# Performance work log

Measured on AMD Instinct MI355X. Metric: run time of the kernel, lower is better.

The kernel has to match this reference:

```python
import jax, jax.numpy as jnp
import numpy as np

GRID = 10
NV = 6
SD = 4
TSD = NV * SD  # 24
PRED = 5
DT = 0.1
BN_EPS = 1e-5


def _conv(x, w, b):
    y = jax.lax.conv_general_dilated(x, w, (1, 1), 'SAME',
                                     dimension_numbers=('NCHW', 'OIHW', 'NCHW'))
    return y + b[None, :, None, None]


def _pool(x):
    return jax.lax.reduce_window(x, -jnp.inf, jax.lax.max,
                                 (1, 1, 2, 2), (1, 1, 2, 2), 'VALID')


def _bn_eval(x, g, b):
    # eval-mode BatchNorm with running_mean=0, running_var=1
    return g * x / jnp.sqrt(1.0 + BN_EPS) + b


def _lstm(x, Wih, Whh, bih, bhh):
    # x: [B, T, D]; torch gate order i, f, g, o
    B = x.shape[0]
    H = Whh.shape[1]
    def step(carry, xt):
        h, c = carry
        gates = xt @ Wih.T + h @ Whh.T + bih + bhh
        i, f, g, o = jnp.split(gates, 4, axis=-1)
        c = jax.nn.sigmoid(f) * c + jax.nn.sigmoid(i) * jnp.tanh(g)
        h = jax.nn.sigmoid(o) * jnp.tanh(c)
        return (h, c), h
    init = (jnp.zeros((B, H), x.dtype), jnp.zeros((B, H), x.dtype))
    (h, c), ys = jax.lax.scan(step, init, jnp.swapaxes(x, 0, 1))
    return jnp.swapaxes(ys, 0, 1), (h, c)


def setup_inputs() -> dict:
    key = jax.random.key(0)
    B, T, D = 512, 100, 400
    C = D // (GRID * GRID)  # 4
    H = 32
    ks = iter(jax.random.split(key, 64))
    r = lambda shape, s=0.1: (s * jax.random.normal(next(ks), shape)).astype(jnp.float32)
    inp = {
        'observations': jax.random.normal(next(ks), (B, T, D), dtype=jnp.float32),
        # CNN
        'c1w': r((16, C, 3, 3)), 'c1b': r((16,)),
        'c2w': r((32, 16, 3, 3)), 'c2b': r((32,)),
        # FCN  (cnn_output_size = 32 * 2 * 2 = 128)
        'f1w': r((128, 128)), 'f1b': r((128,)),
        'bn1g': jnp.ones((128,), jnp.float32), 'bn1b': jnp.zeros((128,), jnp.float32),
        'f2w': r((64, 128)), 'f2b': r((64,)),
        'bn2g': jnp.ones((64,), jnp.float32), 'bn2b': jnp.zeros((64,), jnp.float32),
        # encoder / decoder LSTMs
        'eWih': r((4 * H, 64)), 'eWhh': r((4 * H, H)), 'ebih': r((4 * H,)), 'ebhh': r((4 * H,)),
        'dWih': r((4 * H, H)), 'dWhh': r((4 * H, H)), 'dbih': r((4 * H,)), 'dbhh': r((4 * H,)),
        'ow': r((2 * NV, H)), 'ob': r((2 * NV,)),
        # filter-layer noise LSTMs + FCs
        'qWih': r((4 * H, TSD)), 'qWhh': r((4 * H, H)), 'qbih': r((4 * H,)), 'qbhh': r((4 * H,)),
        'qfw': r((TSD, H)), 'qfb': r((TSD,)),
        'rWih': r((4 * H, TSD)), 'rWhh': r((4 * H, H)), 'rbih': r((4 * H,)), 'rbhh': r((4 * H,)),
        'rfw': r((TSD, H)), 'rfb': r((TSD,)),
    }
    return inp


def _forward(observations, c1w, c1b, c2w, c2b, f1w, f1b, bn1g, bn1b, f2w, f2b,
             bn2g, bn2b, eWih, eWhh, ebih, ebhh, dWih, dWhh, dbih, dbhh, ow, ob,
             qWih, qWhh, qbih, qbhh, qfw, qfb, rWih, rWhh, rbih, rbhh, rfw, rfb):
    B, T, D = observations.shape
    C = c1w.shape[1]
    # ---- InteractionLayer: CNN over all timesteps at once ----
    x = observations.reshape(B * T, C, GRID, GRID)
    x = _pool(jax.nn.relu(_conv(x, c1w, c1b)))   # [B*T,16,5,5]
    x = _pool(jax.nn.relu(_conv(x, c2w, c2b)))   # [B*T,32,2,2]
    x = x.reshape(B * T, -1)                      # [B*T,128]
    x = jax.nn.relu(_bn_eval(x @ f1w.T + f1b, bn1g, bn1b))
    x = jax.nn.relu(_bn_eval(x @ f2w.T + f2b, bn2g, bn2b))  # [B*T,64]
    feats = x.reshape(B, T, 64)
    enc_out, (dh, dc) = _lstm(feats, eWih, eWhh, ebih, ebhh)
    din = enc_out[:, -1]
    preds = []
    for _ in range(PRED):
        gates = din @ dWih.T + dh @ dWhh.T + dbih + dbhh
        i, f, g, o = jnp.split(gates, 4, axis=-1)
        dc = jax.nn.sigmoid(f) * dc + jax.nn.sigmoid(i) * jnp.tanh(g)
        dh = jax.nn.sigmoid(o) * jnp.tanh(dc)
        preds.append(dh @ ow.T + ob)
        din = dh
    accel = jnp.stack(preds, axis=1)  # [B, PRED, 2*NV]
    # ---- MotionLayer (closed-form cumsum kinematics) ----
    init_state = observations[:, -1, :4]
    a = accel.reshape(B, PRED, NV, 2)
    v0 = jnp.zeros((B, NV, 2), jnp.float32).at[:, 0].set(init_state[:, 2:4])
    p0 = jnp.zeros((B, NV, 2), jnp.float32).at[:, 0].set(init_state[:, :2])
    v = v0[:, None] + DT * jnp.cumsum(a, axis=1)
    disp = v * DT + 0.5 * a * DT * DT
    p = p0[:, None] + jnp.cumsum(disp, axis=1)
    traj = jnp.concatenate([p, v], axis=-1).reshape(B, PRED, TSD)
    # ---- FilterLayer: learned noise + Kalman scan ----
    qo, _ = _lstm(traj, qWih, qWhh, qbih, qbhh)
    Qm = jax.vmap(jnp.diag)(jnp.abs(qo[:, -1] @ qfw.T + qfb))  # [B,24,24]
    ro, _ = _lstm(traj, rWih, rWhh, rbih, rbhh)
    Rm = jax.vmap(jnp.diag)(jnp.abs(ro[:, -1] @ rfw.T + rfb))
    Fb = jnp.array([[1, 0, DT, 0], [0, 1, 0, DT], [0, 0, 1, 0], [0, 0, 0, 1]], jnp.float32)
    Fm = jnp.kron(jnp.eye(NV, dtype=jnp.float32), Fb)  # [24,24]
    I = jnp.eye(TSD, dtype=jnp.float32)
    s0 = jnp.zeros((B, TSD), jnp.float32).at[:, :4].set(init_state)
    P0 = jnp.broadcast_to(I, (B, TSD, TSD)) + jnp.zeros((B, TSD, TSD), jnp.float32)
    def kf_step(carry, z):
        s, P = carry
        s_m = s @ Fm.T
        P_m = jnp.einsum('ij,bjk,lk->bil', Fm, P, Fm) + Qm
        S = P_m + Rm
        Kt = jnp.linalg.solve(S, jnp.swapaxes(P_m, 1, 2))
        K = jnp.swapaxes(Kt, 1, 2)
        s_new = s_m + jnp.einsum('bij,bj->bi', K, z - s_m)
        P_new = jnp.einsum('bij,bjk->bik', I - K, P_m)
        return (s_new, P_new), s_new
    _, filt = jax.lax.scan(kf_step, (s0, P0), jnp.swapaxes(traj, 0, 1))
    return jnp.swapaxes(filt, 0, 1)  # [B, PRED, 24]


def reference(observations, c1w, c1b, c2w, c2b, f1w, f1b, bn1g, bn1b, f2w, f2b,
              bn2g, bn2b, eWih, eWhh, ebih, ebhh, dWih, dWhh, dbih, dbhh, ow, ob,
              qWih, qWhh, qbih, qbhh, qfw, qfb, rWih, rWhh, rbih, rbhh, rfw, rfb):
    return _forward(observations, c1w, c1b, c2w, c2b, f1w, f1b, bn1g, bn1b,
                    f2w, f2b, bn2g, bn2b, eWih, eWhh, ebih, ebhh, dWih, dWhh,
                    dbih, dbhh, ow, ob, qWih, qWhh, qbih, qbhh, qfw, qfb,
                    rWih, rWhh, rbih, rbhh, rfw, rfb)
```

## Files before the change

kernel.cpp:

```cpp
#include <hip/hip_runtime.h>

#define BT 51200
#define NB 512

#define P1_OFF   ((size_t)0)
#define X_OFF    ((size_t)20480000)
#define GX_OFF   ((size_t)0)

__device__ __forceinline__ float sigf(float x) {
  return __fdividef(1.f, 1.f + __expf(-x));
}
__device__ __forceinline__ float tanhf2(float x) {
  float ax = fabsf(x);
  float e = __expf(-2.f * ax);
  float r = __fdividef(1.f - e, 1.f + e);
  return x < 0.f ? -r : r;
}
__device__ __forceinline__ float rl(float v, int l) {
  return __uint_as_float(__builtin_amdgcn_readlane(__float_as_uint(v), l));
}

__global__ __launch_bounds__(512, 1)
void k1_conv1_exp(const float* __restrict__ obs, const float* __restrict__ w,
                  const float* __restrict__ bias, float* __restrict__ p1) {
  __shared__ float xs[32 * 411];
  __shared__ float wsh[16 * 36];
  int tid = threadIdx.x;
  int phys = blockIdx.x;
  int x8 = phys & 7;
  int rest = phys >> 3;
  int half = rest & 1;
  int pair = (rest >> 1) * 8 + x8;
  int i0 = pair * 64 + half * 32;
  for (int idx = tid; idx < 12800; idx += 512) {
    int item = idx / 400, feat = idx - item * 400;
    xs[item * 411 + feat] = obs[(size_t)(i0 + item) * 400 + feat];
  }
  for (int idx = tid; idx < 576; idx += 512) wsh[idx] = w[idx];
  __syncthreads();
  int lane = tid & 63;
  int item = lane & 31;
  int oc = (tid >> 6) * 2 + (lane >> 5);
  const float* xrow = xs + item * 411;

#define LOADR(R, C, RR) do { \
  int r_ = 2 * p - 1 + (RR); \
  R[0] = 0.f; R[11] = 0.f; \
  if (r_ >= 0 && r_ <= 9) { \
    _Pragma("unroll") \
    for (int j = 0; j < 10; ++j) R[j + 1] = xrow[(C) * 100 + r_ * 10 + j]; \
  } else { \
    _Pragma("unroll") \
    for (int j = 0; j < 10; ++j) R[j + 1] = 0.f; \
  } \
} while (0)

#define FMAU(II, RA, RB, RC, C) do { \
  const float* wp_ = wsh + oc * 36 + (C) * 9; \
  float w0_ = wp_[0], w1_ = wp_[1], w2_ = wp_[2]; \
  float w3_ = wp_[3], w4_ = wp_[4], w5_ = wp_[5]; \
  float w6_ = wp_[6], w7_ = wp_[7], w8_ = wp_[8]; \
  _Pragma("unroll") \
  for (int q = 0; q < 5; ++q) { \
    _Pragma("unroll") \
    for (int jj = 0; jj < 2; ++jj) { \
      int cb = 2 * q + jj; \
      acc[q][II][jj] += RA[cb] * w0_ + RA[cb + 1] * w1_ + RA[cb + 2] * w2_ \
                      + RB[cb] * w3_ + RB[cb + 1] * w4_ + RB[cb + 2] * w5_ \
                      + RC[cb] * w6_ + RC[cb + 1] * w7_ + RC[cb + 2] * w8_; \
    } \
  } \
} while (0)

  float b0 = bias[oc];
#pragma unroll 1
  for (int p = 0; p < 5; ++p) {
    float acc[5][2][2];
#pragma unroll
    for (int q = 0; q < 5; ++q)
#pragma unroll
      for (int ii = 0; ii < 2; ++ii)
#pragma unroll
        for (int jj = 0; jj < 2; ++jj) acc[q][ii][jj] = b0;
    float R0[12], R1[12], R2[12], R3[12], R4[12], R5[12];
    LOADR(R0, 0, 0); LOADR(R1, 0, 1); LOADR(R2, 0, 2);
    LOADR(R3, 0, 3); LOADR(R4, 1, 0);
    FMAU(0, R0, R1, R2, 0);
    LOADR(R5, 1, 1); LOADR(R0, 1, 2);
    FMAU(1, R1, R2, R3, 0);
    LOADR(R1, 1, 3); LOADR(R2, 2, 0);
    FMAU(0, R4, R5, R0, 1);
    LOADR(R3, 2, 1); LOADR(R4, 2, 2);
    FMAU(1, R5, R0, R1, 1);
    LOADR(R5, 2, 3); LOADR(R0, 3, 0);
    FMAU(0, R2, R3, R4, 2);
    LOADR(R1, 3, 1); LOADR(R2, 3, 2);
    FMAU(1, R3, R4, R5, 2);
    LOADR(R3, 3, 3);
    FMAU(0, R0, R1, R2, 3);
    FMAU(1, R1, R2, R3, 3);
#pragma unroll
    for (int q = 0; q < 5; ++q) {
      float m = fmaxf(fmaxf(acc[q][0][0], acc[q][0][1]),
                      fmaxf(acc[q][1][0], acc[q][1][1]));
      m = fmaxf(m, 0.f);
      p1[(size_t)(oc * 25 + p * 5 + q) * BT + i0 + item] = m;
    }
  }
#undef LOADR
#undef FMAU
}

__global__ __attribute__((amdgpu_flat_work_group_size(1024, 1024)))
__attribute__((amdgpu_waves_per_eu(4, 4)))
void k1_conv1_big(const float* __restrict__ obs, const float* __restrict__ w,
                  const float* __restrict__ bias, float* __restrict__ p1) {
  __shared__ float xs[64 * 401];
  int tid = threadIdx.x;
  int i0 = blockIdx.x * 64;
  for (int idx = tid; idx < 25600; idx += 1024) {
    int item = idx / 400, feat = idx - item * 400;
    xs[item * 401 + feat] = obs[(size_t)(i0 + item) * 400 + feat];
  }
  __syncthreads();
  int lane = tid & 63;
  int wv = __builtin_amdgcn_readfirstlane(tid >> 6);
  const float* xrow = xs + lane * 401;

#define LOADR(R, C, RR) do { \
  int r_ = 2 * p - 1 + (RR); \
  R[0] = 0.f; R[11] = 0.f; \
  if (r_ >= 0 && r_ <= 9) { \
    _Pragma("unroll") \
    for (int j = 0; j < 10; ++j) R[j + 1] = xrow[(C) * 100 + r_ * 10 + j]; \
  } else { \
    _Pragma("unroll") \
    for (int j = 0; j < 10; ++j) R[j + 1] = 0.f; \
  } \
} while (0)

#define FMAU(II, RA, RB, RC, C) do { \
  const float* wa_ = w + wv * 36 + (C) * 9; \
  _Pragma("unroll") \
  for (int q = 0; q < 5; ++q) { \
    _Pragma("unroll") \
    for (int jj = 0; jj < 2; ++jj) { \
      int cb = 2 * q + jj; \
      acc[q][II][jj] += RA[cb] * wa_[0] + RA[cb + 1] * wa_[1] + RA[cb + 2] * wa_[2] \
                      + RB[cb] * wa_[3] + RB[cb + 1] * wa_[4] + RB[cb + 2] * wa_[5] \
                      + RC[cb] * wa_[6] + RC[cb + 1] * wa_[7] + RC[cb + 2] * wa_[8]; \
    } \
  } \
} while (0)

  float b0 = bias[wv];
#pragma unroll 1
  for (int p = 0; p < 5; ++p) {
    float acc[5][2][2];
#pragma unroll
    for (int q = 0; q < 5; ++q)
#pragma unroll
      for (int ii = 0; ii < 2; ++ii)
#pragma unroll
        for (int jj = 0; jj < 2; ++jj) acc[q][ii][jj] = b0;
    float R0[12], R1[12], R2[12], R3[12], R4[12], R5[12];
    LOADR(R0, 0, 0); LOADR(R1, 0, 1); LOADR(R2, 0, 2);
    LOADR(R3, 0, 3); LOADR(R4, 1, 0);
    FMAU(0, R0, R1, R2, 0);
    LOADR(R5, 1, 1); LOADR(R0, 1, 2);
    FMAU(1, R1, R2, R3, 0);
    LOADR(R1, 1, 3); LOADR(R2, 2, 0);
    FMAU(0, R4, R5, R0, 1);
    LOADR(R3, 2, 1); LOADR(R4, 2, 2);
    FMAU(1, R5, R0, R1, 1);
    LOADR(R5, 2, 3); LOADR(R0, 3, 0);
    FMAU(0, R2, R3, R4, 2);
    LOADR(R1, 3, 1); LOADR(R2, 3, 2);
    FMAU(1, R3, R4, R5, 2);
    LOADR(R3, 3, 3);
    FMAU(0, R0, R1, R2, 3);
    FMAU(1, R1, R2, R3, 3);
#pragma unroll
    for (int q = 0; q < 5; ++q) {
      float m = fmaxf(fmaxf(acc[q][0][0], acc[q][0][1]),
                      fmaxf(acc[q][1][0], acc[q][1][1]));
      m = fmaxf(m, 0.f);
      p1[(size_t)(wv * 25 + p * 5 + q) * BT + i0 + lane] = m;
    }
  }
#undef LOADR
#undef FMAU
}

__global__ __launch_bounds__(256, 2)
void k2_conv2(const float* __restrict__ p1, const float* __restrict__ w,
              const float* __restrict__ bias, float* __restrict__ x) {
  int bid = blockIdx.x;
  int inner = bid >> 3;
  int oc = inner & 3;
  int g = ((inner >> 2) << 3) | (bid & 7);
  int item = g * 256 + threadIdx.x;
  float acc[8][16];
#pragma unroll
  for (int o = 0; o < 8; ++o) {
    float bv = bias[oc * 8 + o];
#pragma unroll
    for (int pos = 0; pos < 16; ++pos) acc[o][pos] = bv;
  }
#pragma unroll 1
  for (int c = 0; c < 16; ++c) {
    float in[6][6];
#pragma unroll
    for (int t = 0; t < 6; ++t) { in[0][t] = 0.f; in[t][0] = 0.f; }
#pragma unroll
    for (int i = 0; i < 5; ++i)
#pragma unroll
      for (int j = 0; j < 5; ++j)
        in[i + 1][j + 1] = p1[(size_t)(c * 25 + i * 5 + j) * BT + item];
#pragma unroll
    for (int o = 0; o < 8; ++o) {
#pragma unroll
      for (int i = 0; i < 4; ++i)
#pragma unroll
        for (int j = 0; j < 4; ++j) {
          float a = acc[o][i * 4 + j];
#pragma unroll
          for (int dr = 0; dr < 3; ++dr)
#pragma unroll
            for (int dj = 0; dj < 3; ++dj)
              a += in[i + dr][j + dj] * w[((oc * 8 + o) * 16 + c) * 9 + dr * 3 + dj];
          acc[o][i * 4 + j] = a;
        }
    }
  }
#pragma unroll
  for (int o = 0; o < 8; ++o)
#pragma unroll
    for (int p = 0; p < 2; ++p)
#pragma unroll
      for (int q = 0; q < 2; ++q) {
        float m = fmaxf(fmaxf(acc[o][(2 * p) * 4 + 2 * q], acc[o][(2 * p) * 4 + 2 * q + 1]),
                        fmaxf(acc[o][(2 * p + 1) * 4 + 2 * q], acc[o][(2 * p + 1) * 4 + 2 * q + 1]));
        m = fmaxf(m, 0.f);
        x[(size_t)((oc * 8 + o) * 4 + p * 2 + q) * BT + item] = m;
      }
}

__global__ __launch_bounds__(512, 1)
void k3_fc(const float* __restrict__ x,
           const float* __restrict__ f1w, const float* __restrict__ f1b,
           const float* __restrict__ bn1g, const float* __restrict__ bn1b,
           const float* __restrict__ f2w, const float* __restrict__ f2b,
           const float* __restrict__ bn2g, const float* __restrict__ bn2b,
           const float* __restrict__ eWih, const float* __restrict__ ebih,
           const float* __restrict__ ebhh, float* __restrict__ gx) {
  __shared__ float xs[128 * 64];
  __shared__ float ys[64 * 129];
  const float BNRS = 0.9999950000374997f;
  int tid = threadIdx.x;
  int lane = tid & 63;
  int wv = __builtin_amdgcn_readfirstlane(tid >> 6);
  int i0 = blockIdx.x * 64;
  for (int idx = tid; idx < 8192; idx += 512) {
    int k = idx >> 6, l = idx & 63;
    xs[k * 64 + l] = x[(size_t)k * BT + i0 + l];
  }
  __syncthreads();
#pragma unroll 1
  for (int jj = 0; jj < 4; ++jj) {
    int j0 = wv * 16 + jj * 4;
    float a[4] = {0.f, 0.f, 0.f, 0.f};
#pragma unroll 8
    for (int k = 0; k < 128; ++k) {
      float xv = xs[k * 64 + lane];
#pragma unroll
      for (int u = 0; u < 4; ++u) a[u] += xv * f1w[(j0 + u) * 128 + k];
    }
#pragma unroll
    for (int u = 0; u < 4; ++u) {
      int j = j0 + u;
      float v = a[u] + f1b[j];
      v = bn1g[j] * v * BNRS + bn1b[j];
      ys[j * 64 + lane] = fmaxf(v, 0.f);
    }
  }
  __syncthreads();
#pragma unroll 1
  for (int jj = 0; jj < 2; ++jj) {
    int j0 = wv * 8 + jj * 4;
    float a[4] = {0.f, 0.f, 0.f, 0.f};
#pragma unroll 8
    for (int k = 0; k < 128; ++k) {
      float yv = ys[k * 64 + lane];
#pragma unroll
      for (int u = 0; u < 4; ++u) a[u] += yv * f2w[(j0 + u) * 128 + k];
    }
#pragma unroll
    for (int u = 0; u < 4; ++u) {
      int j = j0 + u;
      float v = a[u] + f2b[j];
      v = bn2g[j] * v * BNRS + bn2b[j];
      xs[j * 64 + lane] = fmaxf(v, 0.f);
    }
  }
  __syncthreads();
#pragma unroll 1
  for (int jj = 0; jj < 4; ++jj) {
    int j0 = wv * 16 + jj * 4;
    float a[4] = {0.f, 0.f, 0.f, 0.f};
#pragma unroll 8
    for (int k = 0; k < 64; ++k) {
      float zv = xs[k * 64 + lane];
#pragma unroll
      for (int u = 0; u < 4; ++u) a[u] += zv * eWih[(j0 + u) * 64 + k];
    }
#pragma unroll
    for (int u = 0; u < 4; ++u) {
      int j = j0 + u;
      ys[lane * 129 + j] = a[u] + ebih[j] + ebhh[j];
    }
  }
  __syncthreads();
  for (int idx = tid; idx < 8192; idx += 512) {
    int item = idx >> 7, j = idx & 127;
    gx[(size_t)(i0 + item) * 128 + j] = ys[item * 129 + j];
  }
}

__global__ __launch_bounds__(128, 2)
void k456(const float* __restrict__ obs, const float* __restrict__ gx,
          const float* __restrict__ eWhh,
          const float* __restrict__ dWih, const float* __restrict__ dWhh,
          const float* __restrict__ dbih, const float* __restrict__ dbhh,
          const float* __restrict__ ow, const float* __restrict__ ob,
          const float* __restrict__ qWih, const float* __restrict__ qWhh,
          const float* __restrict__ qbih, const float* __restrict__ qbhh,
          const float* __restrict__ qfw, const float* __restrict__ qfb,
          const float* __restrict__ rWih, const float* __restrict__ rWhh,
          const float* __restrict__ rbih, const float* __restrict__ rbhh,
          const float* __restrict__ rfw, const float* __restrict__ rfb,
          float* __restrict__ out) {
  __shared__ float arena[8064];
  __shared__ float tL2[2 * 120];
  int tid = threadIdx.x;
  int lane = tid & 63, w = tid >> 6;
  int b = blockIdx.x * 2 + w;
  float* tL = tL2 + w * 120;
  int xl = (lane & 31) + 32;
  int l12 = lane < 12 ? lane : 0;
  int l24 = lane < 24 ? lane : 0;

  float wA[32], wB[32];
#pragma unroll
  for (int k = 0; k < 32; ++k) {
    wA[k] = eWhh[lane * 32 + k];
    wB[k] = eWhh[(lane + 64) * 32 + k];
  }
  float cc = 0.f, hh = 0.f;
  size_t base0 = (size_t)b * 100;
  float ga_n = gx[(base0) * 128 + lane];
  float gb_n = gx[(base0) * 128 + 64 + lane];
#pragma unroll 1
  for (int t = 0; t < 100; ++t) {
    float ga = ga_n, gb2 = gb_n;
    if (t < 99) {
      ga_n = gx[(base0 + t + 1) * 128 + lane];
      gb_n = gx[(base0 + t + 1) * 128 + 64 + lane];
    }
#pragma unroll
    for (int k = 0; k < 32; ++k) {
      float hk = rl(hh, k);
      ga += hk * wA[k];
      gb2 += hk * wB[k];
    }
    float gaX = __shfl(ga, xl);
    float gbX = __shfl(gb2, xl);
    if (lane < 32) {
      float ig = sigf(ga), fg = sigf(gaX);
      float gg = tanhf2(gb2), og = sigf(gbX);
      cc = fg * cc + ig * gg;
      hh = og * tanhf2(cc);
    }
  }

  __syncthreads();
  for (int idx = tid; idx < 4096; idx += 128) {
    int k = idx >> 7, g = idx & 127;
    arena[idx] = dWih[g * 32 + k] + dWhh[g * 32 + k];
  }
  for (int idx = tid; idx < 384; idx += 128) {
    int k = idx / 12, j = idx - k * 12;
    arena[4096 + idx] = ow[j * 32 + k];
  }
  for (int idx = tid; idx < 128; idx += 128)
    arena[4480 + idx] = dbih[idx] + dbhh[idx];
  __syncthreads();
  {
    const float* dwT = arena;
    const float* owT = arena + 4096;
    const float* dbs = arena + 4480;
    float aReg[5];
#pragma unroll 1
    for (int s = 0; s < 5; ++s) {
      float ga = dbs[lane], gb2 = dbs[lane + 64];
#pragma unroll
      for (int k = 0; k < 32; ++k) {
        float hk = rl(hh, k);
        ga += hk * dwT[k * 128 + lane];
        gb2 += hk * dwT[k * 128 + lane + 64];
      }
      float gaX = __shfl(ga, xl);
      float gbX = __shfl(gb2, xl);
      if (lane < 32) {
        float ig = sigf(ga), fg = sigf(gaX);
        float gg = tanhf2(gb2), og = sigf(gbX);
        cc = fg * cc + ig * gg;
        hh = og * tanhf2(cc);
      }
      float pa = ob[l12];
#pragma unroll
      for (int k = 0; k < 32; ++k) pa += rl(hh, k) * owT[k * 12 + l12];
      aReg[s] = pa;
    }
    if (lane < 12) {
      int n = lane >> 1, d = lane & 1;
      float v0 = 0.f, p0 = 0.f;
      if (n == 0) {
        p0 = obs[(size_t)b * 40000 + 39600 + d];
        v0 = obs[(size_t)b * 40000 + 39600 + 2 + d];
      }
      float vc = v0, pc = p0;
#pragma unroll
      for (int s = 0; s < 5; ++s) {
        float a = aReg[s];
        vc += 0.1f * a;
        pc += vc * 0.1f + a * 0.005f;
        tL[s * 24 + n * 4 + d] = pc;
        tL[s * 24 + n * 4 + 2 + d] = vc;
      }
    }
  }

  float qdiag = 0.f, rdiag = 0.f;
#pragma unroll 1
  for (int qr = 0; qr < 2; ++qr) {
    __syncthreads();
    const float* Wih = qr ? rWih : qWih;
    const float* Whh = qr ? rWhh : qWhh;
    const float* bih = qr ? rbih : qbih;
    const float* bhh = qr ? rbhh : qbhh;
    const float* fw  = qr ? rfw  : qfw;
    const float* fb  = qr ? rfb  : qfb;
    for (int idx = tid; idx < 3072; idx += 128) {
      int k = idx >> 7, g = idx & 127;
      arena[idx] = Wih[g * 24 + k];
    }
    for (int idx = tid; idx < 4096; idx += 128) {
      int k = idx >> 7, g = idx & 127;
      arena[3072 + idx] = Whh[g * 32 + k];
    }
    for (int idx = tid; idx < 768; idx += 128) {
      int k = idx / 24, j = idx - k * 24;
      arena[7168 + idx] = fw[j * 32 + k];
    }
    for (int idx = tid; idx < 128; idx += 128)
      arena[7936 + idx] = bih[idx] + bhh[idx];
    __syncthreads();
    const float* ihT = arena;
    const float* hhT = arena + 3072;
    const float* fwT = arena + 7168;
    const float* bs  = arena + 7936;
    hh = 0.f;
    cc = 0.f;
#pragma unroll 1
    for (int s = 0; s < 5; ++s) {
      float ga = bs[lane], gb2 = bs[lane + 64];
#pragma unroll
      for (int k = 0; k < 24; ++k) {
        float z = tL[s * 24 + k];
        ga += z * ihT[k * 128 + lane];
        gb2 += z * ihT[k * 128 + lane + 64];
      }
#pragma unroll
      for (int k = 0; k < 32; ++k) {
        float hk = rl(hh, k);
        ga += hk * hhT[k * 128 + lane];
        gb2 += hk * hhT[k * 128 + lane + 64];
      }
      float gaX = __shfl(ga, xl);
      float gbX = __shfl(gb2, xl);
      if (lane < 32) {
        float ig = sigf(ga), fg = sigf(gaX);
        float gg = tanhf2(gb2), og = sigf(gbX);
        cc = fg * cc + ig * gg;
        hh = og * tanhf2(cc);
      }
    }
    float qv = fb[l24];
#pragma unroll
    for (int k = 0; k < 32; ++k) qv += rl(hh, k) * fwT[k * 24 + l24];
    if (qr == 0) qdiag = fabsf(qv); else rdiag = fabsf(qv);
  }

  {
    float sv = 0.f, qv = 0.f, rv = 0.f;
    if (lane < 24) {
      sv = (lane < 4) ? obs[(size_t)b * 40000 + 39600 + lane] : 0.f;
      qv = qdiag;
      rv = rdiag;
    }
    float p[24];
#pragma unroll
    for (int i = 0; i < 24; ++i) p[i] = (i == lane) ? 1.f : 0.f;
    const int srcPF = ((lane & 3) < 2) ? (lane + 2) : lane;
    const int srcA = (lane < 24) ? lane : (lane - 24);
#pragma unroll 1
    for (int s = 0; s < 5; ++s) {
      float sshift = __shfl(sv, srcPF);
      float smv = sv + (((lane & 3) < 2) ? 0.1f * sshift : 0.f);
#pragma unroll
      for (int i = 0; i < 24; ++i)
        if ((i & 3) < 2) p[i] += 0.1f * p[i + 2];
#pragma unroll
      for (int i = 0; i < 24; ++i) {
        float t = __shfl(p[i], srcPF);
        if ((lane & 3) < 2) p[i] += 0.1f * t;
      }
#pragma unroll
      for (int i = 0; i < 24; ++i) p[i] += (i == lane) ? qv : 0.f;
      float a[24];
#pragma unroll
      for (int i = 0; i < 24; ++i) {
        float t = __shfl(p[i], srcA);
        a[i] = (lane < 24) ? (p[i] + ((i == lane) ? rv : 0.f)) : t;
      }
#pragma unroll
      for (int k = 0; k < 24; ++k) {
        float piv = rl(a[k], k);
        float inv = 1.f / piv;
        float t = a[k] * inv;
#pragma unroll
        for (int i = 0; i < 24; ++i) {
          if (i != k) {
            float fi = rl(a[i], k);
            a[i] = fmaf(-fi, t, a[i]);
          }
        }
        a[k] = t;
      }
      float zv = tL[s * 24 + l24];
      float innv = zv - smv;
      float acc = 0.f;
#pragma unroll
      for (int m = 0; m < 24; ++m) acc += a[m] * rl(innv, m);
      float kupd = __shfl(acc, 24 + l24);
      sv = smv + kupd;
      if (lane < 24) out[(size_t)b * 120 + s * 24 + lane] = sv;
      float pn[24];
#pragma unroll
      for (int i = 0; i < 24; ++i) {
        float acc2 = 0.f;
#pragma unroll
        for (int k = 0; k < 24; ++k) acc2 += rl(a[k], 24 + i) * p[k];
        pn[i] = p[i] - acc2;
      }
#pragma unroll
      for (int i = 0; i < 24; ++i) p[i] = pn[i];
    }
  }
}

extern "C" void kernel_launch(void* const* d_in, const int* in_sizes, int n_in,
                              void* d_out, int out_size, void* d_ws, size_t ws_size,
                              hipStream_t stream) {
  (void)in_sizes; (void)n_in; (void)out_size; (void)ws_size;
  const float* obs  = (const float*)d_in[0];
  const float* c1w  = (const float*)d_in[1];
  const float* c1b  = (const float*)d_in[2];
  const float* c2w  = (const float*)d_in[3];
  const float* c2b  = (const float*)d_in[4];
  const float* f1w  = (const float*)d_in[5];
  const float* f1b  = (const float*)d_in[6];
  const float* bn1g = (const float*)d_in[7];
  const float* bn1b = (const float*)d_in[8];
  const float* f2w  = (const float*)d_in[9];
  const float* f2b  = (const float*)d_in[10];
  const float* bn2g = (const float*)d_in[11];
  const float* bn2b = (const float*)d_in[12];
  const float* eWih = (const float*)d_in[13];
  const float* eWhh = (const float*)d_in[14];
  const float* ebih = (const float*)d_in[15];
  const float* ebhh = (const float*)d_in[16];
  const float* dWih = (const float*)d_in[17];
  const float* dWhh = (const float*)d_in[18];
  const float* dbih = (const float*)d_in[19];
  const float* dbhh = (const float*)d_in[20];
  const float* ow   = (const float*)d_in[21];
  const float* ob   = (const float*)d_in[22];
  const float* qWih = (const float*)d_in[23];
  const float* qWhh = (const float*)d_in[24];
  const float* qbih = (const float*)d_in[25];
  const float* qbhh = (const float*)d_in[26];
  const float* qfw  = (const float*)d_in[27];
  const float* qfb  = (const float*)d_in[28];
  const float* rWih = (const float*)d_in[29];
  const float* rWhh = (const float*)d_in[30];
  const float* rbih = (const float*)d_in[31];
  const float* rbhh = (const float*)d_in[32];
  const float* rfw  = (const float*)d_in[33];
  const float* rfb  = (const float*)d_in[34];

  float* ws = (float*)d_ws;
  float* p1   = ws + P1_OFF;
  float* x    = ws + X_OFF;
  float* gx   = ws + GX_OFF;
  float* out  = (float*)d_out;

  static int k1_use_exp = -1;
  if (k1_use_exp < 0) {
    hipFuncAttributes attr;
    hipError_t e = hipFuncGetAttributes(&attr, (const void*)k1_conv1_exp);
    k1_use_exp = (e == hipSuccess && attr.numRegs >= 100) ? 1 : 0;
  }
  if (k1_use_exp)
    k1_conv1_exp<<<1600, 512, 0, stream>>>(obs, c1w, c1b, p1);
  else
    k1_conv1_big<<<800, 1024, 0, stream>>>(obs, c1w, c1b, p1);

  k2_conv2<<<800, 256, 0, stream>>>(p1, c2w, c2b, x);
  k3_fc<<<800, 512, 0, stream>>>(x, f1w, f1b, bn1g, bn1b, f2w, f2b, bn2g, bn2b,
                                 eWih, ebih, ebhh, gx);
  k456<<<256, 128, 0, stream>>>(obs, gx, eWhh,
                                dWih, dWhh, dbih, dbhh, ow, ob,
                                qWih, qWhh, qbih, qbhh, qfw, qfb,
                                rWih, rWhh, rbih, rbhh, rfw, rfb,
                                out);
}
```

Measured before the change: 590.0 us.

## Stage conv2 inputs and weights in LDS, split output channels across threads

conv2 now loads a 16-item tile of all 400 pooled conv1 values into shared memory, plus a transposed copy of the weights. Each thread computes 2 output channels for one item instead of 8 channels, so 3200 blocks launch instead of 800. This cuts per-thread register pressure and spreads the work over more waves, at the cost of more LDS traffic and a block-wide sync. Separately, the encoder LSTM loop now prefetches the precomputed input gates two steps ahead instead of one, to hide global load latency.

Result: faster. 574.9 us (-2.6%).

```diff
diff --git a/kernel.cpp b/kernel.cpp
--- a/kernel.cpp
+++ b/kernel.cpp
@@ -195,17 +195,33 @@
 __global__ __launch_bounds__(256, 2)
 void k2_conv2(const float* __restrict__ p1, const float* __restrict__ w,
               const float* __restrict__ bias, float* __restrict__ x) {
-  int bid = blockIdx.x;
-  int inner = bid >> 3;
-  int oc = inner & 3;
-  int g = ((inner >> 2) << 3) | (bid & 7);
-  int item = g * 256 + threadIdx.x;
-  float acc[8][16];
-#pragma unroll
-  for (int o = 0; o < 8; ++o) {
-    float bv = bias[oc * 8 + o];
-#pragma unroll
-    for (int pos = 0; pos < 16; ++pos) acc[o][pos] = bv;
+  __shared__ float tile[400 * 16];
+  __shared__ float wT[144 * 33];
+  int tid = threadIdx.x;
+  int phys = blockIdx.x;
+  int x8 = phys & 7;
+  int rest = phys >> 3;
+  int half = rest & 1;
+  int pair = (rest >> 1) * 8 + x8;
+  int i0 = pair * 32 + half * 16;
+  for (int idx = tid; idx < 6400; idx += 256) {
+    int row = idx >> 4, item = idx & 15;
+    tile[row * 16 + item] = p1[(size_t)row * BT + i0 + item];
+  }
+  for (int idx = tid; idx < 4608; idx += 256) {
+    int oc = idx & 31, ct = idx >> 5;
+    wT[ct * 33 + oc] = w[(size_t)(oc * 16 + (ct / 9)) * 9 + (ct % 9)];
+  }
+  __syncthreads();
+  int item = tid & 15;
+  int slot = tid >> 4;
+  const float* trow = tile + item;
+  float acc[2][16];
+#pragma unroll
+  for (int u = 0; u < 2; ++u) {
+    float bv = bias[slot * 2 + u];
+#pragma unroll
+    for (int pos = 0; pos < 16; ++pos) acc[u][pos] = bv;
   }
 #pragma unroll 1
   for (int c = 0; c < 16; ++c) {
@@ -216,34 +232,37 @@
     for (int i = 0; i < 5; ++i)
 #pragma unroll
       for (int j = 0; j < 5; ++j)
-        in[i + 1][j + 1] = p1[(size_t)(c * 25 + i * 5 + j) * BT + item];
-#pragma unroll
-    for (int o = 0; o < 8; ++o) {
+        in[i + 1][j + 1] = trow[(c * 25 + i * 5 + j) * 16];
+#pragma unroll
+    for (int u = 0; u < 2; ++u) {
+      int oc = slot * 2 + u;
 #pragma unroll
       for (int i = 0; i < 4; ++i)
 #pragma unroll
         for (int j = 0; j < 4; ++j) {
-          float a = acc[o][i * 4 + j];
+          float a = acc[u][i * 4 + j];
 #pragma unroll
           for (int dr = 0; dr < 3; ++dr)
 #pragma unroll
             for (int dj = 0; dj < 3; ++dj)
-              a += in[i + dr][j + dj] * w[((oc * 8 + o) * 16 + c) * 9 + dr * 3 + dj];
-          acc[o][i * 4 + j] = a;
+              a += in[i + dr][j + dj] * wT[(c * 9 + dr * 3 + dj) * 33 + oc];
+          acc[u][i * 4 + j] = a;
         }
     }
   }
 #pragma unroll
-  for (int o = 0; o < 8; ++o)
+  for (int u = 0; u < 2; ++u) {
+    int oc = slot * 2 + u;
 #pragma unroll
     for (int p = 0; p < 2; ++p)
 #pragma unroll
       for (int q = 0; q < 2; ++q) {
-        float m = fmaxf(fmaxf(acc[o][(2 * p) * 4 + 2 * q], acc[o][(2 * p) * 4 + 2 * q + 1]),
-                        fmaxf(acc[o][(2 * p + 1) * 4 + 2 * q], acc[o][(2 * p + 1) * 4 + 2 * q + 1]));
+        float m = fmaxf(fmaxf(acc[u][(2 * p) * 4 + 2 * q], acc[u][(2 * p) * 4 + 2 * q + 1]),
+                        fmaxf(acc[u][(2 * p + 1) * 4 + 2 * q], acc[u][(2 * p + 1) * 4 + 2 * q + 1]));
         m = fmaxf(m, 0.f);
-        x[(size_t)((oc * 8 + o) * 4 + p * 2 + q) * BT + item] = m;
-      }
+        x[(size_t)(oc * 4 + p * 2 + q) * BT + i0 + item] = m;
+      }
+  }
 }
 
 __global__ __launch_bounds__(512, 1)
@@ -358,14 +377,17 @@
   }
   float cc = 0.f, hh = 0.f;
   size_t base0 = (size_t)b * 100;
-  float ga_n = gx[(base0) * 128 + lane];
-  float gb_n = gx[(base0) * 128 + 64 + lane];
+  float gaP1 = gx[(base0 + 0) * 128 + lane];
+  float gbP1 = gx[(base0 + 0) * 128 + 64 + lane];
+  float gaP2 = gx[(base0 + 1) * 128 + lane];
+  float gbP2 = gx[(base0 + 1) * 128 + 64 + lane];
 #pragma unroll 1
   for (int t = 0; t < 100; ++t) {
-    float ga = ga_n, gb2 = gb_n;
-    if (t < 99) {
-      ga_n = gx[(base0 + t + 1) * 128 + lane];
-      gb_n = gx[(base0 + t + 1) * 128 + 64 + lane];
+    float ga = gaP1, gb2 = gbP1;
+    gaP1 = gaP2; gbP1 = gbP2;
+    if (t < 98) {
+      gaP2 = gx[(base0 + t + 2) * 128 + lane];
+      gbP2 = gx[(base0 + t + 2) * 128 + 64 + lane];
     }
 #pragma unroll
     for (int k = 0; k < 32; ++k) {
@@ -627,7 +649,7 @@
   else
     k1_conv1_big<<<800, 1024, 0, stream>>>(obs, c1w, c1b, p1);
 
-  k2_conv2<<<800, 256, 0, stream>>>(p1, c2w, c2b, x);
+  k2_conv2<<<3200, 256, 0, stream>>>(p1, c2w, c2b, x);
   k3_fc<<<800, 512, 0, stream>>>(x, f1w, f1b, bn1g, bn1b, f2w, f2b, bn2g, bn2b,
                                  eWih, ebih, ebhh, gx);
   k456<<<256, 128, 0, stream>>>(obs, gx, eWhh,
```
